# Performance work log

Measured on AMD Instinct MI355X. Metric: run time of the kernel, lower is better.

The kernel has to match this reference:

```python
import jax, jax.numpy as jnp
import numpy as np

TOKENS = 131072
DIM = 512
NUM_EXPERTS = 4
TOPK = 2
ROUTE_SCALE = 1.0


def setup_inputs() -> dict:
    key = jax.random.key(0)
    k1, k2, k3 = jax.random.split(key, 3)
    x = jax.random.normal(k1, (TOKENS, DIM), dtype=jnp.float32)
    weight = jax.random.normal(k2, (NUM_EXPERTS, DIM), dtype=jnp.float32) * 0.02
    bias = jax.random.normal(k3, (NUM_EXPERTS,), dtype=jnp.float32) * 0.01
    return {"x": x, "weight": weight, "bias": bias}


def reference(x, weight, bias):
    # scores = x @ W^T -> [T, E]
    logits = jnp.einsum('td,ed->te', x, weight)
    scores = jax.nn.softmax(logits.astype(jnp.float32), axis=-1)  # fp32 softmax
    biased = scores + bias  # bias only affects expert selection
    _, indices = jax.lax.top_k(biased, TOPK)  # [T, topk] int32
    weights = jnp.take_along_axis(scores, indices, axis=1) * ROUTE_SCALE
    return weights.astype(x.dtype), indices
```

## Files before the change

kernel.cpp:

```cpp
#include <hip/hip_runtime.h>
#include <math.h>


constexpr int TOKENS = 131072;
constexpr int DIM = 512;
constexpr int CHUNK = 16;

typedef float fvec4 __attribute__((ext_vector_type(4)));

__global__ __launch_bounds__(256, 4) void gate_kernel(
    const float* __restrict__ x,
    const float* __restrict__ w,
    const float* __restrict__ bias,
    float* __restrict__ out_w,
    float* __restrict__ out_i)
{
    const int lane = threadIdx.x & 63;
    const int wave = blockIdx.x * (blockDim.x >> 6) + (threadIdx.x >> 6);
    const int t0   = wave * CHUNK;

    const int cLo = 4 * lane;
    const int cHi = 256 + 4 * lane;

    const fvec4 w0a = *reinterpret_cast<const fvec4*>(w + 0 * DIM + cLo);
    const fvec4 w0b = *reinterpret_cast<const fvec4*>(w + 0 * DIM + cHi);
    const fvec4 w1a = *reinterpret_cast<const fvec4*>(w + 1 * DIM + cLo);
    const fvec4 w1b = *reinterpret_cast<const fvec4*>(w + 1 * DIM + cHi);
    const fvec4 w2a = *reinterpret_cast<const fvec4*>(w + 2 * DIM + cLo);
    const fvec4 w2b = *reinterpret_cast<const fvec4*>(w + 2 * DIM + cHi);
    const fvec4 w3a = *reinterpret_cast<const fvec4*>(w + 3 * DIM + cLo);
    const fvec4 w3b = *reinterpret_cast<const fvec4*>(w + 3 * DIM + cHi);
    const float b0 = bias[0], b1 = bias[1], b2 = bias[2], b3 = bias[3];

    #pragma unroll
    for (int j = 0; j < CHUNK; j += 2) {
        const int tA = t0 + j;
        const int tB = tA + 1;
        const float* rowA = x + (size_t)tA * DIM;
        const float* rowB = x + (size_t)tB * DIM;

        const fvec4 xa0 = __builtin_nontemporal_load(reinterpret_cast<const fvec4*>(rowA + cLo));
        const fvec4 xa1 = __builtin_nontemporal_load(reinterpret_cast<const fvec4*>(rowA + cHi));
        const fvec4 xb0 = __builtin_nontemporal_load(reinterpret_cast<const fvec4*>(rowB + cLo));
        const fvec4 xb1 = __builtin_nontemporal_load(reinterpret_cast<const fvec4*>(rowB + cHi));

        float A0 = xa0.x*w0a.x + xa0.y*w0a.y + xa0.z*w0a.z + xa0.w*w0a.w
                 + xa1.x*w0b.x + xa1.y*w0b.y + xa1.z*w0b.z + xa1.w*w0b.w;
        float A1 = xa0.x*w1a.x + xa0.y*w1a.y + xa0.z*w1a.z + xa0.w*w1a.w
                 + xa1.x*w1b.x + xa1.y*w1b.y + xa1.z*w1b.z + xa1.w*w1b.w;
        float A2 = xa0.x*w2a.x + xa0.y*w2a.y + xa0.z*w2a.z + xa0.w*w2a.w
                 + xa1.x*w2b.x + xa1.y*w2b.y + xa1.z*w2b.z + xa1.w*w2b.w;
        float A3 = xa0.x*w3a.x + xa0.y*w3a.y + xa0.z*w3a.z + xa0.w*w3a.w
                 + xa1.x*w3b.x + xa1.y*w3b.y + xa1.z*w3b.z + xa1.w*w3b.w;

        float B0 = xb0.x*w0a.x + xb0.y*w0a.y + xb0.z*w0a.z + xb0.w*w0a.w
                 + xb1.x*w0b.x + xb1.y*w0b.y + xb1.z*w0b.z + xb1.w*w0b.w;
        float B1 = xb0.x*w1a.x + xb0.y*w1a.y + xb0.z*w1a.z + xb0.w*w1a.w
                 + xb1.x*w1b.x + xb1.y*w1b.y + xb1.z*w1b.z + xb1.w*w1b.w;
        float B2 = xb0.x*w2a.x + xb0.y*w2a.y + xb0.z*w2a.z + xb0.w*w2a.w
                 + xb1.x*w2b.x + xb1.y*w2b.y + xb1.z*w2b.z + xb1.w*w2b.w;
        float B3 = xb0.x*w3a.x + xb0.y*w3a.y + xb0.z*w3a.z + xb0.w*w3a.w
                 + xb1.x*w3b.x + xb1.y*w3b.y + xb1.z*w3b.z + xb1.w*w3b.w;

        #pragma unroll
        for (int off = 1; off < 64; off <<= 1) {
            A0 += __shfl_xor(A0, off, 64);
            B0 += __shfl_xor(B0, off, 64);
            A1 += __shfl_xor(A1, off, 64);
            B1 += __shfl_xor(B1, off, 64);
            A2 += __shfl_xor(A2, off, 64);
            B2 += __shfl_xor(B2, off, 64);
            A3 += __shfl_xor(A3, off, 64);
            B3 += __shfl_xor(B3, off, 64);
        }

        float sA0, sA1, sA2, sA3;
        {
            const float m  = fmaxf(fmaxf(A0, A1), fmaxf(A2, A3));
            const float e0 = __expf(A0 - m), e1 = __expf(A1 - m);
            const float e2 = __expf(A2 - m), e3 = __expf(A3 - m);
            const float inv = 1.0f / (e0 + e1 + e2 + e3);
            sA0 = e0 * inv; sA1 = e1 * inv; sA2 = e2 * inv; sA3 = e3 * inv;
        }
        float sB0, sB1, sB2, sB3;
        {
            const float m  = fmaxf(fmaxf(B0, B1), fmaxf(B2, B3));
            const float e0 = __expf(B0 - m), e1 = __expf(B1 - m);
            const float e2 = __expf(B2 - m), e3 = __expf(B3 - m);
            const float inv = 1.0f / (e0 + e1 + e2 + e3);
            sB0 = e0 * inv; sB1 = e1 * inv; sB2 = e2 * inv; sB3 = e3 * inv;
        }

        const float pA0 = sA0 + b0, pA1 = sA1 + b1, pA2 = sA2 + b2, pA3 = sA3 + b3;
        int   iA0 = 0; float bvA = pA0, svA0 = sA0;
        if (pA1 > bvA) { bvA = pA1; svA0 = sA1; iA0 = 1; }
        if (pA2 > bvA) { bvA = pA2; svA0 = sA2; iA0 = 2; }
        if (pA3 > bvA) { bvA = pA3; svA0 = sA3; iA0 = 3; }
        int   iA1 = -1; float bvA1 = -INFINITY, svA1 = 0.0f;
        if (iA0 != 0 && pA0 > bvA1) { bvA1 = pA0; svA1 = sA0; iA1 = 0; }
        if (iA0 != 1 && pA1 > bvA1) { bvA1 = pA1; svA1 = sA1; iA1 = 1; }
        if (iA0 != 2 && pA2 > bvA1) { bvA1 = pA2; svA1 = sA2; iA1 = 2; }
        if (iA0 != 3 && pA3 > bvA1) { bvA1 = pA3; svA1 = sA3; iA1 = 3; }

        const float pB0 = sB0 + b0, pB1 = sB1 + b1, pB2 = sB2 + b2, pB3 = sB3 + b3;
        int   iB0 = 0; float bvB = pB0, svB0 = sB0;
        if (pB1 > bvB) { bvB = pB1; svB0 = sB1; iB0 = 1; }
        if (pB2 > bvB) { bvB = pB2; svB0 = sB2; iB0 = 2; }
        if (pB3 > bvB) { bvB = pB3; svB0 = sB3; iB0 = 3; }
        int   iB1 = -1; float bvB1 = -INFINITY, svB1 = 0.0f;
        if (iB0 != 0 && pB0 > bvB1) { bvB1 = pB0; svB1 = sB0; iB1 = 0; }
        if (iB0 != 1 && pB1 > bvB1) { bvB1 = pB1; svB1 = sB1; iB1 = 1; }
        if (iB0 != 2 && pB2 > bvB1) { bvB1 = pB2; svB1 = sB2; iB1 = 2; }
        if (iB0 != 3 && pB3 > bvB1) { bvB1 = pB3; svB1 = sB3; iB1 = 3; }

        if (lane == 0) {
            fvec4 wv; wv.x = svA0; wv.y = svA1; wv.z = svB0; wv.w = svB1;
            fvec4 iv; iv.x = (float)iA0; iv.y = (float)iA1; iv.z = (float)iB0; iv.w = (float)iB1;
            *reinterpret_cast<fvec4*>(out_w + 2 * (size_t)tA) = wv;
            *reinterpret_cast<fvec4*>(out_i + 2 * (size_t)tA) = iv;
        }
    }
}

extern "C" void kernel_launch(void* const* d_in, const int* in_sizes, int n_in,
                              void* d_out, int out_size, void* d_ws, size_t ws_size,
                              hipStream_t stream) {
    const float* x    = (const float*)d_in[0];
    const float* w    = (const float*)d_in[1];
    const float* bias = (const float*)d_in[2];

    float* out_w = (float*)d_out;
    float* out_i = (float*)d_out + (size_t)TOKENS * 2;

    const int block  = 256;
    const int blocks = TOKENS / (CHUNK * 4);
    gate_kernel<<<blocks, block, 0, stream>>>(x, w, bias, out_w, out_i);
}
```

Baseline: 56.80 us.

## Switch to grid-stride token-pair loop with contiguous per-lane 32-byte loads

Replaces the fixed 16-token chunk per wave with a grid-stride loop over token pairs on a fixed grid of 2048 blocks. Each lane now loads 8 contiguous floats instead of two fvec4s split across half-rows. Nontemporal loads and the occupancy hint in launch_bounds are dropped. The dynamic loop loses full unrolling, so fewer loads are in flight per wave, and the contiguous per-lane layout changes coalescing on a bandwidth-bound 256MB read.

```diff
diff --git a/kernel.cpp b/kernel.cpp
--- a/kernel.cpp
+++ b/kernel.cpp
@@ -4,45 +4,41 @@
 
 constexpr int TOKENS = 131072;
 constexpr int DIM = 512;
-constexpr int CHUNK = 16;
 
 typedef float fvec4 __attribute__((ext_vector_type(4)));
 
-__global__ __launch_bounds__(256, 4) void gate_kernel(
+__global__ __launch_bounds__(256) void gate_kernel(
     const float* __restrict__ x,
     const float* __restrict__ w,
     const float* __restrict__ bias,
     float* __restrict__ out_w,
     float* __restrict__ out_i)
 {
-    const int lane = threadIdx.x & 63;
-    const int wave = blockIdx.x * (blockDim.x >> 6) + (threadIdx.x >> 6);
-    const int t0   = wave * CHUNK;
+    const int lane   = threadIdx.x & 63;
+    const int wavesPerBlock = blockDim.x >> 6;
+    const int wave   = blockIdx.x * wavesPerBlock + (threadIdx.x >> 6);
+    const int nwaves = gridDim.x * wavesPerBlock;
 
-    const int cLo = 4 * lane;
-    const int cHi = 256 + 4 * lane;
-
-    const fvec4 w0a = *reinterpret_cast<const fvec4*>(w + 0 * DIM + cLo);
-    const fvec4 w0b = *reinterpret_cast<const fvec4*>(w + 0 * DIM + cHi);
-    const fvec4 w1a = *reinterpret_cast<const fvec4*>(w + 1 * DIM + cLo);
-    const fvec4 w1b = *reinterpret_cast<const fvec4*>(w + 1 * DIM + cHi);
-    const fvec4 w2a = *reinterpret_cast<const fvec4*>(w + 2 * DIM + cLo);
-    const fvec4 w2b = *reinterpret_cast<const fvec4*>(w + 2 * DIM + cHi);
-    const fvec4 w3a = *reinterpret_cast<const fvec4*>(w + 3 * DIM + cLo);
-    const fvec4 w3b = *reinterpret_cast<const fvec4*>(w + 3 * DIM + cHi);
+    const float4 w0a = *reinterpret_cast<const float4*>(w + 0 * DIM + lane * 8);
+    const float4 w0b = *reinterpret_cast<const float4*>(w + 0 * DIM + lane * 8 + 4);
+    const float4 w1a = *reinterpret_cast<const float4*>(w + 1 * DIM + lane * 8);
+    const float4 w1b = *reinterpret_cast<const float4*>(w + 1 * DIM + lane * 8 + 4);
+    const float4 w2a = *reinterpret_cast<const float4*>(w + 2 * DIM + lane * 8);
+    const float4 w2b = *reinterpret_cast<const float4*>(w + 2 * DIM + lane * 8 + 4);
+    const float4 w3a = *reinterpret_cast<const float4*>(w + 3 * DIM + lane * 8);
+    const float4 w3b = *reinterpret_cast<const float4*>(w + 3 * DIM + lane * 8 + 4);
     const float b0 = bias[0], b1 = bias[1], b2 = bias[2], b3 = bias[3];
 
-    #pragma unroll
-    for (int j = 0; j < CHUNK; j += 2) {
-        const int tA = t0 + j;
+    for (int tp = wave; tp < TOKENS / 2; tp += nwaves) {
+        const int tA = tp * 2;
         const int tB = tA + 1;
-        const float* rowA = x + (size_t)tA * DIM;
-        const float* rowB = x + (size_t)tB * DIM;
+        const float4* pA = reinterpret_cast<const float4*>(x + (size_t)tA * DIM + lane * 8);
+        const float4* pB = reinterpret_cast<const float4*>(x + (size_t)tB * DIM + lane * 8);
 
-        const fvec4 xa0 = __builtin_nontemporal_load(reinterpret_cast<const fvec4*>(rowA + cLo));
-        const fvec4 xa1 = __builtin_nontemporal_load(reinterpret_cast<const fvec4*>(rowA + cHi));
-        const fvec4 xb0 = __builtin_nontemporal_load(reinterpret_cast<const fvec4*>(rowB + cLo));
-        const fvec4 xb1 = __builtin_nontemporal_load(reinterpret_cast<const fvec4*>(rowB + cHi));
+        const float4 xa0 = pA[0];
+        const float4 xa1 = pA[1];
+        const float4 xb0 = pB[0];
+        const float4 xb1 = pB[1];
 
         float A0 = xa0.x*w0a.x + xa0.y*w0a.y + xa0.z*w0a.z + xa0.w*w0a.w
                  + xa1.x*w0b.x + xa1.y*w0b.y + xa1.z*w0b.z + xa1.w*w0b.w;
@@ -91,27 +87,27 @@
             sB0 = e0 * inv; sB1 = e1 * inv; sB2 = e2 * inv; sB3 = e3 * inv;
         }
 
-        const float pA0 = sA0 + b0, pA1 = sA1 + b1, pA2 = sA2 + b2, pA3 = sA3 + b3;
-        int   iA0 = 0; float bvA = pA0, svA0 = sA0;
-        if (pA1 > bvA) { bvA = pA1; svA0 = sA1; iA0 = 1; }
-        if (pA2 > bvA) { bvA = pA2; svA0 = sA2; iA0 = 2; }
-        if (pA3 > bvA) { bvA = pA3; svA0 = sA3; iA0 = 3; }
+        const float pA0s = sA0 + b0, pA1s = sA1 + b1, pA2s = sA2 + b2, pA3s = sA3 + b3;
+        int   iA0 = 0; float bvA = pA0s, svA0 = sA0;
+        if (pA1s > bvA) { bvA = pA1s; svA0 = sA1; iA0 = 1; }
+        if (pA2s > bvA) { bvA = pA2s; svA0 = sA2; iA0 = 2; }
+        if (pA3s > bvA) { bvA = pA3s; svA0 = sA3; iA0 = 3; }
         int   iA1 = -1; float bvA1 = -INFINITY, svA1 = 0.0f;
-        if (iA0 != 0 && pA0 > bvA1) { bvA1 = pA0; svA1 = sA0; iA1 = 0; }
-        if (iA0 != 1 && pA1 > bvA1) { bvA1 = pA1; svA1 = sA1; iA1 = 1; }
-        if (iA0 != 2 && pA2 > bvA1) { bvA1 = pA2; svA1 = sA2; iA1 = 2; }
-        if (iA0 != 3 && pA3 > bvA1) { bvA1 = pA3; svA1 = sA3; iA1 = 3; }
+        if (iA0 != 0 && pA0s > bvA1) { bvA1 = pA0s; svA1 = sA0; iA1 = 0; }
+        if (iA0 != 1 && pA1s > bvA1) { bvA1 = pA1s; svA1 = sA1; iA1 = 1; }
+        if (iA0 != 2 && pA2s > bvA1) { bvA1 = pA2s; svA1 = sA2; iA1 = 2; }
+        if (iA0 != 3 && pA3s > bvA1) { bvA1 = pA3s; svA1 = sA3; iA1 = 3; }
 
-        const float pB0 = sB0 + b0, pB1 = sB1 + b1, pB2 = sB2 + b2, pB3 = sB3 + b3;
-        int   iB0 = 0; float bvB = pB0, svB0 = sB0;
-        if (pB1 > bvB) { bvB = pB1; svB0 = sB1; iB0 = 1; }
-        if (pB2 > bvB) { bvB = pB2; svB0 = sB2; iB0 = 2; }
-        if (pB3 > bvB) { bvB = pB3; svB0 = sB3; iB0 = 3; }
+        const float pB0s = sB0 + b0, pB1s = sB1 + b1, pB2s = sB2 + b2, pB3s = sB3 + b3;
+        int   iB0 = 0; float bvB = pB0s, svB0 = sB0;
+        if (pB1s > bvB) { bvB = pB1s; svB0 = sB1; iB0 = 1; }
+        if (pB2s > bvB) { bvB = pB2s; svB0 = sB2; iB0 = 2; }
+        if (pB3s > bvB) { bvB = pB3s; svB0 = sB3; iB0 = 3; }
         int   iB1 = -1; float bvB1 = -INFINITY, svB1 = 0.0f;
-        if (iB0 != 0 && pB0 > bvB1) { bvB1 = pB0; svB1 = sB0; iB1 = 0; }
-        if (iB0 != 1 && pB1 > bvB1) { bvB1 = pB1; svB1 = sB1; iB1 = 1; }
-        if (iB0 != 2 && pB2 > bvB1) { bvB1 = pB2; svB1 = sB2; iB1 = 2; }
-        if (iB0 != 3 && pB3 > bvB1) { bvB1 = pB3; svB1 = sB3; iB1 = 3; }
+        if (iB0 != 0 && pB0s > bvB1) { bvB1 = pB0s; svB1 = sB0; iB1 = 0; }
+        if (iB0 != 1 && pB1s > bvB1) { bvB1 = pB1s; svB1 = sB1; iB1 = 1; }
+        if (iB0 != 2 && pB2s > bvB1) { bvB1 = pB2s; svB1 = sB2; iB1 = 2; }
+        if (iB0 != 3 && pB3s > bvB1) { bvB1 = pB3s; svB1 = sB3; iB1 = 3; }
 
         if (lane == 0) {
             fvec4 wv; wv.x = svA0; wv.y = svA1; wv.z = svB0; wv.w = svB1;
@@ -133,6 +129,6 @@
     float* out_i = (float*)d_out + (size_t)TOKENS * 2;
 
     const int block  = 256;
-    const int blocks = TOKENS / (CHUNK * 4);
+    const int blocks = 2048;
     gate_kernel<<<blocks, block, 0, stream>>>(x, w, bias, out_w, out_i);
 }
```

Result: faster. 50.13 us (-11.7%).
